# Performance work log

Measured on AMD Instinct MI355X. Metric: run time of the kernel, lower is better.

The kernel has to match this reference:

```python
import jax, jax.numpy as jnp
import numpy as np

USER_NUM = 100000
ITEM_NUM = 50000
N_NODES = USER_NUM + ITEM_NUM
EMB = 128
N_EDGES = 600000
N_LAYERS = 3


def setup_inputs() -> dict:
    key = jax.random.key(0)
    k1, k2, k3, k4, k5 = jax.random.split(key, 5)
    user_emb = jax.random.normal(k1, (USER_NUM, EMB), dtype=jnp.float32) * 0.05
    item_emb = jax.random.normal(k2, (ITEM_NUM, EMB), dtype=jnp.float32) * 0.05
    edge_row = jax.random.randint(k3, (N_EDGES,), 0, N_NODES, dtype=jnp.int32)
    edge_col = jax.random.randint(k4, (N_EDGES,), 0, N_NODES, dtype=jnp.int32)
    # symmetric-normalized adjacency values (positive, ~1/deg scale)
    edge_vals = jax.random.uniform(k5, (N_EDGES,), dtype=jnp.float32) * 0.1
    return {
        "user_emb": user_emb,
        "item_emb": item_emb,
        "edge_vals": edge_vals,
        "edge_row": edge_row,
        "edge_col": edge_col,
    }


def _spmm(edge_vals, edge_row, edge_col, x):
    # torch.sparse.mm(A, x) with A in COO form: out[r] += v * x[c]
    gathered = edge_vals[:, None] * x[edge_col]  # [E, D]
    return jax.ops.segment_sum(gathered, edge_row, num_segments=N_NODES)


def reference(user_emb, item_emb, edge_vals, edge_row, edge_col):
    ego = jnp.concatenate([user_emb, item_emb], axis=0)  # [N, D]
    acc = jnp.zeros_like(ego)
    for _ in range(N_LAYERS):
        ego = _spmm(edge_vals, edge_row, edge_col, ego)
        acc = acc + ego  # fused running sum instead of stack+mean
    all_embeddings = acc / N_LAYERS
    user_all = all_embeddings[:USER_NUM]
    item_all = all_embeddings[USER_NUM:]
    return (user_all, item_all)
```

## Files before the change

### kernel.cpp

```cpp
#include <hip/hip_runtime.h>

constexpr int USER_NUM = 100000;
constexpr int ITEM_NUM = 50000;
constexpr int N_NODES  = USER_NUM + ITEM_NUM;
constexpr int EMB      = 128;
constexpr int N_EDGES  = 600000;
constexpr int SCAN_BS  = 1024;

__device__ __forceinline__ float bf2f(unsigned u16) {
    return __uint_as_float(u16 << 16);
}
__device__ __forceinline__ unsigned f2bf(float f) {
    unsigned u = __float_as_uint(f);
    u += 0x7fffu + ((u >> 16) & 1u);
    return u >> 16;
}
__device__ __forceinline__ void fmadd_bf(float4& s, float v, uint2 g) {
    s.x += v * bf2f(g.x & 0xffffu);
    s.y += v * bf2f(g.x >> 16);
    s.z += v * bf2f(g.y & 0xffffu);
    s.w += v * bf2f(g.y >> 16);
}

__global__ void conv_k(const float4* __restrict__ ue, const float4* __restrict__ ie,
                       uint4* __restrict__ xb) {
    int i = blockIdx.x * 256 + threadIdx.x;
    const int n = N_NODES * EMB / 8;
    if (i >= n) return;
    const int u4 = USER_NUM * EMB / 4;
    int f = 2 * i;
    float4 a, b;
    if (f < u4) { a = ue[f]; b = ue[f + 1]; }
    else        { a = ie[f - u4]; b = ie[f + 1 - u4]; }
    uint4 o;
    o.x = f2bf(a.x) | (f2bf(a.y) << 16);
    o.y = f2bf(a.z) | (f2bf(a.w) << 16);
    o.z = f2bf(b.x) | (f2bf(b.y) << 16);
    o.w = f2bf(b.z) | (f2bf(b.w) << 16);
    xb[i] = o;
}

__global__ void hist_rank_k(const int* __restrict__ er, int* __restrict__ cnt,
                            int* __restrict__ rank) {
    int e = blockIdx.x * 256 + threadIdx.x;
    if (e < N_EDGES) rank[e] = atomicAdd(&cnt[er[e]], 1);
}

__global__ __launch_bounds__(SCAN_BS) void scan_fused_k(
        const int* __restrict__ cnt, int* __restrict__ gcount,
        int2* __restrict__ rowinfo) {
    __shared__ int sh[SCAN_BS];
    __shared__ int sbase;
    int i = blockIdx.x * SCAN_BS + threadIdx.x;
    int v = (i < N_NODES) ? cnt[i] : 0;
    sh[threadIdx.x] = v;
    __syncthreads();
    for (int off = 1; off < SCAN_BS; off <<= 1) {
        int t = (threadIdx.x >= off) ? sh[threadIdx.x - off] : 0;
        __syncthreads();
        sh[threadIdx.x] += t;
        __syncthreads();
    }
    if (threadIdx.x == SCAN_BS - 1)
        sbase = atomicAdd(gcount, sh[SCAN_BS - 1]);
    __syncthreads();
    if (i < N_NODES)
        rowinfo[i] = make_int2(sbase + sh[threadIdx.x] - v, v);
}

__global__ void scatter_k(const int* __restrict__ er, const int* __restrict__ ec,
                          const float* __restrict__ ev, const int* __restrict__ rank,
                          const int2* __restrict__ rowinfo, int2* __restrict__ edges) {
    int e = blockIdx.x * 256 + threadIdx.x;
    if (e >= N_EDGES) return;
    int p = rowinfo[er[e]].x + rank[e];
    edges[p] = make_int2(ec[e], __float_as_int(ev[e]));
}

template <int MODE>
__global__ __launch_bounds__(256) void spmm_gather_bf(
        const uint2* __restrict__ x, const int2* __restrict__ rowinfo,
        const int2* __restrict__ edges, uint2* __restrict__ out,
        const uint2* __restrict__ b0, float4* __restrict__ acc) {
    int row  = blockIdx.x * 8 + (threadIdx.x >> 5);
    int lane = threadIdx.x & 31;
    int2 ri = rowinfo[row];
    int e0 = ri.x, eend = ri.x + ri.y;
    float4 s = make_float4(0.f, 0.f, 0.f, 0.f);
    for (int base = e0; base < eend; base += 4) {
        int i1 = (base + 1 < eend) ? base + 1 : eend - 1;
        int i2 = (base + 2 < eend) ? base + 2 : eend - 1;
        int i3 = (base + 3 < eend) ? base + 3 : eend - 1;
        int2 p0 = edges[base], p1 = edges[i1], p2 = edges[i2], p3 = edges[i3];
        float v0 = __int_as_float(p0.y);
        float v1 = (base + 1 < eend) ? __int_as_float(p1.y) : 0.f;
        float v2 = (base + 2 < eend) ? __int_as_float(p2.y) : 0.f;
        float v3 = (base + 3 < eend) ? __int_as_float(p3.y) : 0.f;
        uint2 g0 = x[(size_t)p0.x * 32 + lane];
        uint2 g1 = x[(size_t)p1.x * 32 + lane];
        uint2 g2 = x[(size_t)p2.x * 32 + lane];
        uint2 g3 = x[(size_t)p3.x * 32 + lane];
        fmadd_bf(s, v0, g0);
        fmadd_bf(s, v1, g1);
        fmadd_bf(s, v2, g2);
        fmadd_bf(s, v3, g3);
    }
    size_t o = (size_t)row * 32 + lane;
    if (MODE < 2) {
        uint2 w;
        w.x = f2bf(s.x) | (f2bf(s.y) << 16);
        w.y = f2bf(s.z) | (f2bf(s.w) << 16);
        out[o] = w;
    } else {
        uint2 a0 = b0[o];
        uint2 a1 = x[o];
        const float k = 1.0f / 3.0f;
        float4 r;
        r.x = (s.x + bf2f(a0.x & 0xffffu) + bf2f(a1.x & 0xffffu)) * k;
        r.y = (s.y + bf2f(a0.x >> 16)     + bf2f(a1.x >> 16))     * k;
        r.z = (s.z + bf2f(a0.y & 0xffffu) + bf2f(a1.y & 0xffffu)) * k;
        r.w = (s.w + bf2f(a0.y >> 16)     + bf2f(a1.y >> 16))     * k;
        acc[o] = r;
    }
}

__global__ void spmm_first_at(const float* __restrict__ ue, const float* __restrict__ ie,
                              const float* __restrict__ ev, const int* __restrict__ er,
                              const int* __restrict__ ec, float* __restrict__ out) {
    int tid = blockIdx.x * blockDim.x + threadIdx.x;
    int edge = tid >> 5;
    if (edge >= N_EDGES) return;
    int lane = tid & 31;
    int row = er[edge]; int col = ec[edge]; float v = ev[edge];
    const float* x = (col < USER_NUM) ? (ue + (size_t)col * EMB)
                                      : (ie + (size_t)(col - USER_NUM) * EMB);
    float4 g = ((const float4*)x)[lane];
    float* o = out + (size_t)row * EMB + lane * 4;
    atomicAdd(o + 0, v * g.x); atomicAdd(o + 1, v * g.y);
    atomicAdd(o + 2, v * g.z); atomicAdd(o + 3, v * g.w);
}
__global__ void spmm_at(const float* __restrict__ x, const float* __restrict__ ev,
                        const int* __restrict__ er, const int* __restrict__ ec,
                        float* __restrict__ out) {
    int tid = blockIdx.x * blockDim.x + threadIdx.x;
    int edge = tid >> 5;
    if (edge >= N_EDGES) return;
    int lane = tid & 31;
    int row = er[edge]; int col = ec[edge]; float v = ev[edge];
    float4 g = ((const float4*)(x + (size_t)col * EMB))[lane];
    float* o = out + (size_t)row * EMB + lane * 4;
    atomicAdd(o + 0, v * g.x); atomicAdd(o + 1, v * g.y);
    atomicAdd(o + 2, v * g.z); atomicAdd(o + 3, v * g.w);
}
__global__ void acc_add(float* __restrict__ acc, const float* __restrict__ cur,
                        float scale, int n4) {
    int i = blockIdx.x * blockDim.x + threadIdx.x;
    if (i >= n4) return;
    float4 a = ((const float4*)acc)[i];
    float4 c = ((const float4*)cur)[i];
    a.x = (a.x + c.x) * scale; a.y = (a.y + c.y) * scale;
    a.z = (a.z + c.z) * scale; a.w = (a.w + c.w) * scale;
    ((float4*)acc)[i] = a;
}

extern "C" void kernel_launch(void* const* d_in, const int* in_sizes, int n_in,
                              void* d_out, int out_size, void* d_ws, size_t ws_size,
                              hipStream_t stream) {
    const float* ue = (const float*)d_in[0];
    const float* ie = (const float*)d_in[1];
    const float* ev = (const float*)d_in[2];
    const int*   er = (const int*)d_in[3];
    const int*   ec = (const int*)d_in[4];
    float* acc = (float*)d_out;

    size_t nnodes32 = (size_t)N_NODES * 32;

    uint2* x0   = (uint2*)d_ws;
    uint2* e1b  = x0 + nnodes32;
    uint2* e2b  = e1b + nnodes32;
    int*   cnt  = (int*)(e2b + nnodes32);
    int*   gcount = cnt + N_NODES;
    int2*  rowinfo = (int2*)(gcount + 1);
    int*   rank = (int*)(rowinfo + N_NODES);
    int2*  edges = (int2*)(rank + N_EDGES);
    size_t needed = (char*)(edges + N_EDGES) - (char*)d_ws;

    const int BLOCK = 256;
    const int eblocks = (N_EDGES + BLOCK - 1) / BLOCK;
    const int nscan = (N_NODES + SCAN_BS - 1) / SCAN_BS;

    if (ws_size >= needed) {
        const int cvt_n = N_NODES * EMB / 8;
        conv_k<<<(cvt_n + BLOCK - 1) / BLOCK, BLOCK, 0, stream>>>(
            (const float4*)ue, (const float4*)ie, (uint4*)x0);

        hipMemsetAsync(cnt, 0, ((size_t)N_NODES + 1) * sizeof(int), stream);
        hist_rank_k<<<eblocks, BLOCK, 0, stream>>>(er, cnt, rank);
        scan_fused_k<<<nscan, SCAN_BS, 0, stream>>>(cnt, gcount, rowinfo);
        scatter_k<<<eblocks, BLOCK, 0, stream>>>(er, ec, ev, rank, rowinfo, edges);

        const int gblocks = N_NODES / 8;
        spmm_gather_bf<0><<<gblocks, BLOCK, 0, stream>>>(
            x0, rowinfo, edges, e1b, nullptr, nullptr);
        spmm_gather_bf<1><<<gblocks, BLOCK, 0, stream>>>(
            e1b, rowinfo, edges, e2b, nullptr, nullptr);
        spmm_gather_bf<2><<<gblocks, BLOCK, 0, stream>>>(
            e2b, rowinfo, edges, nullptr, e1b, (float4*)acc);
    } else {
        size_t nfloats = (size_t)N_NODES * EMB;
        float* buf0 = (float*)d_ws;
        float* buf1 = buf0 + nfloats;
        const int spmm_blocks = (N_EDGES * 32) / BLOCK;
        const int n4 = (int)(nfloats / 4);
        const int add_blocks = (n4 + BLOCK - 1) / BLOCK;
        hipMemsetAsync(acc, 0, nfloats * sizeof(float), stream);
        hipMemsetAsync(buf0, 0, nfloats * sizeof(float), stream);
        spmm_first_at<<<spmm_blocks, BLOCK, 0, stream>>>(ue, ie, ev, er, ec, buf0);
        acc_add<<<add_blocks, BLOCK, 0, stream>>>(acc, buf0, 1.0f, n4);
        hipMemsetAsync(buf1, 0, nfloats * sizeof(float), stream);
        spmm_at<<<spmm_blocks, BLOCK, 0, stream>>>(buf0, ev, er, ec, buf1);
        acc_add<<<add_blocks, BLOCK, 0, stream>>>(acc, buf1, 1.0f, n4);
        hipMemsetAsync(buf0, 0, nfloats * sizeof(float), stream);
        spmm_at<<<spmm_blocks, BLOCK, 0, stream>>>(buf1, ev, er, ec, buf0);
        acc_add<<<add_blocks, BLOCK, 0, stream>>>(acc, buf0, 1.0f / 3.0f, n4);
    }
}
```

Measured before the change: 313.2 us.

## Widen gather loads to 16 bytes, fuse convert with histogram, nontemporal output stores

The SpMM gather kernel now uses 16 lanes per row, each loading uint4 (8 bf16 values), so each block handles 16 rows and each gathered row is fetched with fewer, wider loads. The bf16 conversion and the edge histogram/rank kernels are merged into one launch with block-range dispatch, removing a launch and letting the two phases overlap. The final fp32 output is written with nontemporal stores to avoid polluting cache. More registers per thread and fewer in-flight rows per wave are the trade-offs.

```diff
diff --git a/kernel.cpp b/kernel.cpp
--- a/kernel.cpp
+++ b/kernel.cpp
@@ -7,6 +7,12 @@
 constexpr int N_EDGES  = 600000;
 constexpr int SCAN_BS  = 1024;
 
+constexpr int CVT_N      = N_NODES * EMB / 8;
+constexpr int CVT_BLOCKS = CVT_N / 256;
+constexpr int EBLOCKS    = (N_EDGES + 255) / 256;
+
+typedef float vf4 __attribute__((ext_vector_type(4)));
+
 __device__ __forceinline__ float bf2f(unsigned u16) {
     return __uint_as_float(u16 << 16);
 }
@@ -15,35 +21,39 @@
     u += 0x7fffu + ((u >> 16) & 1u);
     return u >> 16;
 }
-__device__ __forceinline__ void fmadd_bf(float4& s, float v, uint2 g) {
-    s.x += v * bf2f(g.x & 0xffffu);
-    s.y += v * bf2f(g.x >> 16);
-    s.z += v * bf2f(g.y & 0xffffu);
-    s.w += v * bf2f(g.y >> 16);
-}
-
-__global__ void conv_k(const float4* __restrict__ ue, const float4* __restrict__ ie,
-                       uint4* __restrict__ xb) {
-    int i = blockIdx.x * 256 + threadIdx.x;
-    const int n = N_NODES * EMB / 8;
-    if (i >= n) return;
-    const int u4 = USER_NUM * EMB / 4;
-    int f = 2 * i;
-    float4 a, b;
-    if (f < u4) { a = ue[f]; b = ue[f + 1]; }
-    else        { a = ie[f - u4]; b = ie[f + 1 - u4]; }
-    uint4 o;
-    o.x = f2bf(a.x) | (f2bf(a.y) << 16);
-    o.y = f2bf(a.z) | (f2bf(a.w) << 16);
-    o.z = f2bf(b.x) | (f2bf(b.y) << 16);
-    o.w = f2bf(b.z) | (f2bf(b.w) << 16);
-    xb[i] = o;
-}
-
-__global__ void hist_rank_k(const int* __restrict__ er, int* __restrict__ cnt,
-                            int* __restrict__ rank) {
-    int e = blockIdx.x * 256 + threadIdx.x;
-    if (e < N_EDGES) rank[e] = atomicAdd(&cnt[er[e]], 1);
+__device__ __forceinline__ void fmadd_bf8(float* s, float v, uint4 g) {
+    s[0] += v * bf2f(g.x & 0xffffu);
+    s[1] += v * bf2f(g.x >> 16);
+    s[2] += v * bf2f(g.y & 0xffffu);
+    s[3] += v * bf2f(g.y >> 16);
+    s[4] += v * bf2f(g.z & 0xffffu);
+    s[5] += v * bf2f(g.z >> 16);
+    s[6] += v * bf2f(g.w & 0xffffu);
+    s[7] += v * bf2f(g.w >> 16);
+}
+
+__global__ __launch_bounds__(256) void conv_hist_k(
+        const float4* __restrict__ ue, const float4* __restrict__ ie,
+        uint4* __restrict__ xb, const int* __restrict__ er,
+        int* __restrict__ cnt, int* __restrict__ rank) {
+    int b = blockIdx.x;
+    if (b < CVT_BLOCKS) {
+        int i = b * 256 + threadIdx.x;
+        const int u4 = USER_NUM * EMB / 4;
+        int f = 2 * i;
+        float4 a, c;
+        if (f < u4) { a = ue[f]; c = ue[f + 1]; }
+        else        { a = ie[f - u4]; c = ie[f + 1 - u4]; }
+        uint4 o;
+        o.x = f2bf(a.x) | (f2bf(a.y) << 16);
+        o.y = f2bf(a.z) | (f2bf(a.w) << 16);
+        o.z = f2bf(c.x) | (f2bf(c.y) << 16);
+        o.w = f2bf(c.z) | (f2bf(c.w) << 16);
+        xb[i] = o;
+    } else {
+        int e = (b - CVT_BLOCKS) * 256 + threadIdx.x;
+        if (e < N_EDGES) rank[e] = atomicAdd(&cnt[er[e]], 1);
+    }
 }
 
 __global__ __launch_bounds__(SCAN_BS) void scan_fused_k(
@@ -79,14 +89,14 @@
 
 template <int MODE>
 __global__ __launch_bounds__(256) void spmm_gather_bf(
-        const uint2* __restrict__ x, const int2* __restrict__ rowinfo,
-        const int2* __restrict__ edges, uint2* __restrict__ out,
-        const uint2* __restrict__ b0, float4* __restrict__ acc) {
-    int row  = blockIdx.x * 8 + (threadIdx.x >> 5);
-    int lane = threadIdx.x & 31;
+        const uint4* __restrict__ x, const int2* __restrict__ rowinfo,
+        const int2* __restrict__ edges, uint4* __restrict__ out,
+        const uint4* __restrict__ b0, float* __restrict__ acc) {
+    int row  = blockIdx.x * 16 + (threadIdx.x >> 4);
+    int lane = threadIdx.x & 15;
     int2 ri = rowinfo[row];
     int e0 = ri.x, eend = ri.x + ri.y;
-    float4 s = make_float4(0.f, 0.f, 0.f, 0.f);
+    float s[8] = {0.f, 0.f, 0.f, 0.f, 0.f, 0.f, 0.f, 0.f};
     for (int base = e0; base < eend; base += 4) {
         int i1 = (base + 1 < eend) ? base + 1 : eend - 1;
         int i2 = (base + 2 < eend) ? base + 2 : eend - 1;
@@ -96,31 +106,39 @@
         float v1 = (base + 1 < eend) ? __int_as_float(p1.y) : 0.f;
         float v2 = (base + 2 < eend) ? __int_as_float(p2.y) : 0.f;
         float v3 = (base + 3 < eend) ? __int_as_float(p3.y) : 0.f;
-        uint2 g0 = x[(size_t)p0.x * 32 + lane];
-        uint2 g1 = x[(size_t)p1.x * 32 + lane];
-        uint2 g2 = x[(size_t)p2.x * 32 + lane];
-        uint2 g3 = x[(size_t)p3.x * 32 + lane];
-        fmadd_bf(s, v0, g0);
-        fmadd_bf(s, v1, g1);
-        fmadd_bf(s, v2, g2);
-        fmadd_bf(s, v3, g3);
-    }
-    size_t o = (size_t)row * 32 + lane;
+        uint4 g0 = x[(size_t)p0.x * 16 + lane];
+        uint4 g1 = x[(size_t)p1.x * 16 + lane];
+        uint4 g2 = x[(size_t)p2.x * 16 + lane];
+        uint4 g3 = x[(size_t)p3.x * 16 + lane];
+        fmadd_bf8(s, v0, g0);
+        fmadd_bf8(s, v1, g1);
+        fmadd_bf8(s, v2, g2);
+        fmadd_bf8(s, v3, g3);
+    }
+    size_t o = (size_t)row * 16 + lane;
     if (MODE < 2) {
-        uint2 w;
-        w.x = f2bf(s.x) | (f2bf(s.y) << 16);
-        w.y = f2bf(s.z) | (f2bf(s.w) << 16);
+        uint4 w;
+        w.x = f2bf(s[0]) | (f2bf(s[1]) << 16);
+        w.y = f2bf(s[2]) | (f2bf(s[3]) << 16);
+        w.z = f2bf(s[4]) | (f2bf(s[5]) << 16);
+        w.w = f2bf(s[6]) | (f2bf(s[7]) << 16);
         out[o] = w;
     } else {
-        uint2 a0 = b0[o];
-        uint2 a1 = x[o];
+        uint4 a0 = b0[o];
+        uint4 a1 = x[o];
         const float k = 1.0f / 3.0f;
-        float4 r;
-        r.x = (s.x + bf2f(a0.x & 0xffffu) + bf2f(a1.x & 0xffffu)) * k;
-        r.y = (s.y + bf2f(a0.x >> 16)     + bf2f(a1.x >> 16))     * k;
-        r.z = (s.z + bf2f(a0.y & 0xffffu) + bf2f(a1.y & 0xffffu)) * k;
-        r.w = (s.w + bf2f(a0.y >> 16)     + bf2f(a1.y >> 16))     * k;
-        acc[o] = r;
+        vf4 r0, r1;
+        r0.x = (s[0] + bf2f(a0.x & 0xffffu) + bf2f(a1.x & 0xffffu)) * k;
+        r0.y = (s[1] + bf2f(a0.x >> 16)     + bf2f(a1.x >> 16))     * k;
+        r0.z = (s[2] + bf2f(a0.y & 0xffffu) + bf2f(a1.y & 0xffffu)) * k;
+        r0.w = (s[3] + bf2f(a0.y >> 16)     + bf2f(a1.y >> 16))     * k;
+        r1.x = (s[4] + bf2f(a0.z & 0xffffu) + bf2f(a1.z & 0xffffu)) * k;
+        r1.y = (s[5] + bf2f(a0.z >> 16)     + bf2f(a1.z >> 16))     * k;
+        r1.z = (s[6] + bf2f(a0.w & 0xffffu) + bf2f(a1.w & 0xffffu)) * k;
+        r1.w = (s[7] + bf2f(a0.w >> 16)     + bf2f(a1.w >> 16))     * k;
+        vf4* dst = reinterpret_cast<vf4*>(acc) + (size_t)row * 32 + (size_t)lane * 2;
+        __builtin_nontemporal_store(r0, dst);
+        __builtin_nontemporal_store(r1, dst + 1);
     }
 }
 
@@ -173,12 +191,12 @@
     const int*   ec = (const int*)d_in[4];
     float* acc = (float*)d_out;
 
-    size_t nnodes32 = (size_t)N_NODES * 32;
-
-    uint2* x0   = (uint2*)d_ws;
-    uint2* e1b  = x0 + nnodes32;
-    uint2* e2b  = e1b + nnodes32;
-    int*   cnt  = (int*)(e2b + nnodes32);
+    size_t nnodes16 = (size_t)N_NODES * 16;
+
+    uint4* x0   = (uint4*)d_ws;
+    uint4* e1b  = x0 + nnodes16;
+    uint4* e2b  = e1b + nnodes16;
+    int*   cnt  = (int*)(e2b + nnodes16);
     int*   gcount = cnt + N_NODES;
     int2*  rowinfo = (int2*)(gcount + 1);
     int*   rank = (int*)(rowinfo + N_NODES);
@@ -186,26 +204,22 @@
     size_t needed = (char*)(edges + N_EDGES) - (char*)d_ws;
 
     const int BLOCK = 256;
-    const int eblocks = (N_EDGES + BLOCK - 1) / BLOCK;
     const int nscan = (N_NODES + SCAN_BS - 1) / SCAN_BS;
 
     if (ws_size >= needed) {
-        const int cvt_n = N_NODES * EMB / 8;
-        conv_k<<<(cvt_n + BLOCK - 1) / BLOCK, BLOCK, 0, stream>>>(
-            (const float4*)ue, (const float4*)ie, (uint4*)x0);
-
-        hipMemsetAsync(cnt, 0, ((size_t)N_NODES + 1) * sizeof(int), stream);
-        hist_rank_k<<<eblocks, BLOCK, 0, stream>>>(er, cnt, rank);
+        (void)hipMemsetAsync(cnt, 0, ((size_t)N_NODES + 1) * sizeof(int), stream);
+        conv_hist_k<<<CVT_BLOCKS + EBLOCKS, BLOCK, 0, stream>>>(
+            (const float4*)ue, (const float4*)ie, x0, er, cnt, rank);
         scan_fused_k<<<nscan, SCAN_BS, 0, stream>>>(cnt, gcount, rowinfo);
-        scatter_k<<<eblocks, BLOCK, 0, stream>>>(er, ec, ev, rank, rowinfo, edges);
-
-        const int gblocks = N_NODES / 8;
+        scatter_k<<<EBLOCKS, BLOCK, 0, stream>>>(er, ec, ev, rank, rowinfo, edges);
+
+        const int gblocks = N_NODES / 16;
         spmm_gather_bf<0><<<gblocks, BLOCK, 0, stream>>>(
             x0, rowinfo, edges, e1b, nullptr, nullptr);
         spmm_gather_bf<1><<<gblocks, BLOCK, 0, stream>>>(
             e1b, rowinfo, edges, e2b, nullptr, nullptr);
         spmm_gather_bf<2><<<gblocks, BLOCK, 0, stream>>>(
-            e2b, rowinfo, edges, nullptr, e1b, (float4*)acc);
+            e2b, rowinfo, edges, nullptr, e1b, acc);
     } else {
         size_t nfloats = (size_t)N_NODES * EMB;
         float* buf0 = (float*)d_ws;
@@ -213,14 +227,14 @@
         const int spmm_blocks = (N_EDGES * 32) / BLOCK;
         const int n4 = (int)(nfloats / 4);
         const int add_blocks = (n4 + BLOCK - 1) / BLOCK;
-        hipMemsetAsync(acc, 0, nfloats * sizeof(float), stream);
-        hipMemsetAsync(buf0, 0, nfloats * sizeof(float), stream);
+        (void)hipMemsetAsync(acc, 0, nfloats * sizeof(float), stream);
+        (void)hipMemsetAsync(buf0, 0, nfloats * sizeof(float), stream);
         spmm_first_at<<<spmm_blocks, BLOCK, 0, stream>>>(ue, ie, ev, er, ec, buf0);
         acc_add<<<add_blocks, BLOCK, 0, stream>>>(acc, buf0, 1.0f, n4);
-        hipMemsetAsync(buf1, 0, nfloats * sizeof(float), stream);
+        (void)hipMemsetAsync(buf1, 0, nfloats * sizeof(float), stream);
         spmm_at<<<spmm_blocks, BLOCK, 0, stream>>>(buf0, ev, er, ec, buf1);
         acc_add<<<add_blocks, BLOCK, 0, stream>>>(acc, buf1, 1.0f, n4);
-        hipMemsetAsync(buf0, 0, nfloats * sizeof(float), stream);
+        (void)hipMemsetAsync(buf0, 0, nfloats * sizeof(float), stream);
         spmm_at<<<spmm_blocks, BLOCK, 0, stream>>>(buf1, ev, er, ec, buf0);
         acc_add<<<add_blocks, BLOCK, 0, stream>>>(acc, buf0, 1.0f / 3.0f, n4);
     }
```

Result: faster. 299.2 us (-4.5%).
